# Kernel tuning notes

Measured on AMD Instinct MI355X. Metric: run time of the kernel, lower is better.

Reference implementation:

```python
import jax, jax.numpy as jnp
import numpy as np

DIM = 1024
NUM_HEADS = 16
HEAD_DIM = DIM // NUM_HEADS
SCALE = HEAD_DIM ** -0.5


def setup_inputs() -> dict:
    key = jax.random.key(0)
    ks = jax.random.split(key, 7)
    b, n = 2, 2048
    x = jax.random.normal(ks[0], (b, n, DIM), dtype=jnp.float32)
    s = DIM ** -0.5
    Wq = jax.random.normal(ks[1], (DIM, DIM), dtype=jnp.float32) * s
    bq = jax.random.normal(ks[2], (DIM,), dtype=jnp.float32) * 0.01
    Wk = jax.random.normal(ks[3], (DIM, DIM), dtype=jnp.float32) * s
    bk = jax.random.normal(ks[4], (DIM,), dtype=jnp.float32) * 0.01
    Wv = jax.random.normal(ks[5], (DIM, DIM), dtype=jnp.float32) * s
    bv = jax.random.normal(ks[6], (DIM,), dtype=jnp.float32) * 0.01
    return {"x": x, "Wq": Wq, "bq": bq, "Wk": Wk, "bk": bk, "Wv": Wv, "bv": bv}


def reference(x, Wq, bq, Wk, bk, Wv, bv):
    b, n, _ = x.shape
    # Linear projections (torch Linear: x @ W.T + b; here W stored as [in, out])
    q = x @ Wq + bq
    k = x @ Wk + bk
    v = x @ Wv + bv
    # split heads: [b, n, h*d] -> [b, h, n, d]
    split = lambda t: t.reshape(b, n, NUM_HEADS, HEAD_DIM).transpose(0, 2, 1, 3)
    q, k, v = split(q), split(k), split(v)
    sim = jnp.einsum('bhid,bhjd->bhij', q, k) * SCALE
    attn = jax.nn.softmax(sim, axis=-1)
    out = jnp.einsum('bhij,bhjd->bhid', attn, v)
    return out.transpose(0, 2, 1, 3).reshape(b, n, DIM)
```

## Files before the change

### kernel.cpp

```cpp
#include <hip/hip_runtime.h>
#include <cstdint>
#include <cstddef>

#define NB    2
#define SEQ   2048
#define DIMC  1024
#define NH    16
#define HDIM  64
#define MROWS (NB*SEQ)
#define NFEAT (3*DIMC)
#define KVBLK 64
#define NT    (SEQ/KVBLK)

typedef _Float16 half8 __attribute__((ext_vector_type(8)));
typedef _Float16 half4 __attribute__((ext_vector_type(4)));
typedef _Float16 half2v __attribute__((ext_vector_type(2)));
typedef __fp16   fp16x2 __attribute__((ext_vector_type(2)));
typedef float    f32x4 __attribute__((ext_vector_type(4)));

typedef const __attribute__((address_space(1))) void* gas_ptr;
typedef __attribute__((address_space(3))) void*       las_ptr;

__device__ __forceinline__ void gload_lds16(const void* g, void* l) {
    __builtin_amdgcn_global_load_lds((gas_ptr)g, (las_ptr)l, 16, 0, 0);
}

__device__ __forceinline__ int swz4(int r) { return (r ^ (r >> 2)) & 3; }

__device__ __forceinline__ float fast_exp2(float x) {
    float r;
    asm("v_exp_f32 %0, %1" : "=v"(r) : "v"(x));
    return r;
}

__device__ __forceinline__ half2v pk_f16(float a, float b) {
    fp16x2 r = __builtin_amdgcn_cvt_pkrtz(a, b);
    return __builtin_bit_cast(half2v, r);
}

__global__ __launch_bounds__(256) void k_convert_x(const float* __restrict__ x,
                                                   _Float16* __restrict__ x16) {
    int i = (blockIdx.x * 256 + threadIdx.x) * 4;
    float4 v = *reinterpret_cast<const float4*>(x + i);
    half4 h = { (_Float16)v.x, (_Float16)v.y, (_Float16)v.z, (_Float16)v.w };
    *reinterpret_cast<half4*>(x16 + i) = h;
}

__global__ __launch_bounds__(256) void k_transpose_w(const float* __restrict__ Wq,
                                                     const float* __restrict__ Wk,
                                                     const float* __restrict__ Wv,
                                                     _Float16* __restrict__ wt) {
    __shared__ float tile[64][65];
    const int bid  = blockIdx.x;
    const int midx = bid >> 8;
    const int t2   = bid & 255;
    const int i0   = (t2 >> 4) * 64;
    const int o0   = (t2 & 15) * 64;
    const float* W = (midx == 0) ? Wq : (midx == 1 ? Wk : Wv);
    const int tid  = threadIdx.x;
    #pragma unroll
    for (int p = 0; p < 4; ++p) {
        int id = p * 256 + tid;
        int r = id >> 4, c4 = (id & 15) * 4;
        float4 v = *reinterpret_cast<const float4*>(W + (size_t)(i0 + r) * DIMC + o0 + c4);
        tile[r][c4 + 0] = v.x; tile[r][c4 + 1] = v.y;
        tile[r][c4 + 2] = v.z; tile[r][c4 + 3] = v.w;
    }
    __syncthreads();
    #pragma unroll
    for (int p = 0; p < 4; ++p) {
        int id = p * 256 + tid;
        int oc = id >> 4, i4 = (id & 15) * 4;
        half4 h = { (_Float16)tile[i4 + 0][oc], (_Float16)tile[i4 + 1][oc],
                    (_Float16)tile[i4 + 2][oc], (_Float16)tile[i4 + 3][oc] };
        *reinterpret_cast<half4*>(wt + (size_t)(midx * DIMC + o0 + oc) * DIMC + i0 + i4) = h;
    }
}

__global__ __launch_bounds__(256) void k_qkv_gemm(
    const _Float16* __restrict__ x16, const _Float16* __restrict__ wt,
    const float* __restrict__ bq, const float* __restrict__ bk, const float* __restrict__ bv,
    _Float16* __restrict__ q16, _Float16* __restrict__ k16, _Float16* __restrict__ vt16)
{
    __shared__ __align__(16) char sraw[34816];
    const int tid = threadIdx.x;
    const int lane = tid & 63;
    const int w = tid >> 6, wm = w >> 1, wn = w & 1;
    const int lr = lane & 15, lg = lane >> 4;
    const int bn = blockIdx.x % (NFEAT / 128);
    const int bm = blockIdx.x / (NFEAT / 128);
    const int m0 = bm * 128, n0 = bn * 128;

    const f32x4 zero4 = {0.f, 0.f, 0.f, 0.f};
    f32x4 acc[4][4];
    #pragma unroll
    for (int i = 0; i < 4; ++i)
        #pragma unroll
        for (int j = 0; j < 4; ++j) acc[i][j] = zero4;

    auto stage = [&](int buf, int kt) {
        const int k0 = kt * 32;
        char* Adst = sraw + buf * 8192;
        char* Bdst = sraw + 16384 + buf * 8192;
        #pragma unroll
        for (int t = 0; t < 2; ++t) {
            int slot = t * 256 + tid;
            int row = slot >> 2, ch = slot & 3;
            int chg = ch ^ swz4(row);
            gload_lds16(x16 + (size_t)(m0 + row) * DIMC + k0 + chg * 8, Adst + slot * 16);
            gload_lds16(wt  + (size_t)(n0 + row) * DIMC + k0 + chg * 8, Bdst + slot * 16);
        }
    };

    stage(0, 0);
    for (int kt = 0; kt < DIMC / 32; ++kt) {
        __syncthreads();
        if (kt + 1 < DIMC / 32) stage((kt + 1) & 1, kt + 1);
        const char* Ab = sraw + (kt & 1) * 8192;
        const char* Bb = sraw + 16384 + (kt & 1) * 8192;
        half8 af[4], bf[4];
        #pragma unroll
        for (int mb = 0; mb < 4; ++mb) {
            int row = wm * 64 + mb * 16 + lr;
            af[mb] = *(const half8*)(Ab + row * 64 + ((lg ^ swz4(row)) << 4));
        }
        #pragma unroll
        for (int nb = 0; nb < 4; ++nb) {
            int col = wn * 64 + nb * 16 + lr;
            bf[nb] = *(const half8*)(Bb + col * 64 + ((lg ^ swz4(col)) << 4));
        }
        #pragma unroll
        for (int mb = 0; mb < 4; ++mb)
            #pragma unroll
            for (int nb = 0; nb < 4; ++nb)
                acc[mb][nb] = __builtin_amdgcn_mfma_f32_16x16x32_f16(af[mb], bf[nb], acc[mb][nb], 0, 0, 0);
    }

    const int sec = n0 >> 10;
    const float* bias = (sec == 0) ? bq : (sec == 1 ? bk : bv);
    const float scl = (sec == 0) ? 0.125f * 1.44269504088896f : 1.0f;
    float bfv[4];
    #pragma unroll
    for (int nb = 0; nb < 4; ++nb)
        bfv[nb] = bias[(n0 & 1023) + wn * 64 + nb * 16 + lr];

    if (sec < 2) {
        _Float16* dst = (sec == 0) ? q16 : k16;
        #pragma unroll
        for (int mb = 0; mb < 4; ++mb)
            #pragma unroll
            for (int i2 = 0; i2 < 4; ++i2) {
                int rg = m0 + wm * 64 + mb * 16 + lg * 4 + i2;
                int bb = rg >> 11, nn = rg & (SEQ - 1);
                #pragma unroll
                for (int nb = 0; nb < 4; ++nb) {
                    int f1 = (n0 & 1023) + wn * 64 + nb * 16 + lr;
                    int hh = f1 >> 6, dd = f1 & 63;
                    dst[((size_t)(bb * NH + hh) * SEQ + nn) * HDIM + dd] =
                        (_Float16)((acc[mb][nb][i2] + bfv[nb]) * scl);
                }
            }
    } else {
        __syncthreads();
        char* lt = sraw;
        #pragma unroll
        for (int mb = 0; mb < 4; ++mb)
            #pragma unroll
            for (int nb = 0; nb < 4; ++nb) {
                int c  = wn * 64 + nb * 16 + lr;
                int r0 = wm * 64 + mb * 16 + lg * 4;
                half4 hv = { (_Float16)(acc[mb][nb][0] + bfv[nb]),
                             (_Float16)(acc[mb][nb][1] + bfv[nb]),
                             (_Float16)(acc[mb][nb][2] + bfv[nb]),
                             (_Float16)(acc[mb][nb][3] + bfv[nb]) };
                *(half4*)(lt + c * 272 + r0 * 2) = hv;
            }
        __syncthreads();
        #pragma unroll
        for (int p = 0; p < 8; ++p) {
            int id = p * 256 + tid;
            int c = id >> 4, r8 = (id & 15) * 8;
            half8 hv = *(const half8*)(lt + c * 272 + r8 * 2);
            int f1 = (n0 & 1023) + c;
            int hh = f1 >> 6, dd = f1 & 63;
            int rg = m0 + r8;
            int bb = rg >> 11, nn = rg & (SEQ - 1);
            *(half8*)(vt16 + ((size_t)(bb * NH + hh) * HDIM + dd) * SEQ + nn) = hv;
        }
    }
}

__global__ __launch_bounds__(256) void k_attn(
    const _Float16* __restrict__ q16, const _Float16* __restrict__ k16,
    const _Float16* __restrict__ vt16, float* __restrict__ out)
{
    __shared__ __align__(16) char lds[49152];
    const int tid = threadIdx.x, lane = tid & 63, w = tid >> 6;
    const int lr = lane & 15, lg = lane >> 4;
    const int swz = (blockIdx.x & 7) * 64 + (blockIdx.x >> 3);
    const int bh = swz >> 4;
    const int qt = swz & 15;
    const int qrow0 = qt * 128 + w * 32;
    const _Float16* qh = q16 + (size_t)bh * SEQ * HDIM;
    const _Float16* kh = k16 + (size_t)bh * SEQ * HDIM;
    const _Float16* vh = vt16 + (size_t)bh * HDIM * SEQ;
    char* pl = lds + 32768 + w * 4096;
    const int rb = lr >> 3;

    auto stageKV = [&](int buf, int j0) {
        #pragma unroll
        for (int t = 0; t < 2; ++t) {
            int slot = t * 256 + tid;
            int row  = slot >> 3;
            int chg  = (slot & 7) ^ (row & 7);
            gload_lds16(kh + (size_t)(j0 + row) * HDIM + chg * 8,
                        lds + buf * 8192 + slot * 16);
            gload_lds16(vh + (size_t)row * SEQ + j0 + chg * 8,
                        lds + 16384 + buf * 8192 + slot * 16);
        }
    };

    half8 aq[2][2];
    #pragma unroll
    for (int g = 0; g < 2; ++g)
        #pragma unroll
        for (int kc = 0; kc < 2; ++kc)
            aq[g][kc] = *(const half8*)(qh + (size_t)(qrow0 + g * 16 + lr) * HDIM + kc * 32 + lg * 8);

    const f32x4 zero4 = {0.f, 0.f, 0.f, 0.f};
    f32x4 l4[2] = { zero4, zero4 };
    f32x4 oacc[2][4];
    #pragma unroll
    for (int g = 0; g < 2; ++g)
        #pragma unroll
        for (int i = 0; i < 4; ++i) oacc[g][i] = zero4;

    stageKV(0, 0);
    for (int t = 0; t < NT; ++t) {
        const int j0 = t * KVBLK;
        __syncthreads();
        if (t + 1 < NT) stageKV((t + 1) & 1, j0 + KVBLK);
        const char* Kb = lds + (t & 1) * 8192;
        const char* Vb = lds + 16384 + (t & 1) * 8192;

        f32x4 s[2][4];
        __builtin_amdgcn_s_setprio(1);
        #pragma unroll
        for (int jb = 0; jb < 4; ++jb) {
            int row = jb * 16 + lr;
            half8 k0 = *(const half8*)(Kb + row * 128 + (((0 + lg) ^ (row & 7)) << 4));
            half8 k1 = *(const half8*)(Kb + row * 128 + (((4 + lg) ^ (row & 7)) << 4));
            f32x4 sa0 = zero4, sa1 = zero4;
            sa0 = __builtin_amdgcn_mfma_f32_16x16x32_f16(k0, aq[0][0], sa0, 0, 0, 0);
            sa1 = __builtin_amdgcn_mfma_f32_16x16x32_f16(k0, aq[1][0], sa1, 0, 0, 0);
            sa0 = __builtin_amdgcn_mfma_f32_16x16x32_f16(k1, aq[0][1], sa0, 0, 0, 0);
            sa1 = __builtin_amdgcn_mfma_f32_16x16x32_f16(k1, aq[1][1], sa1, 0, 0, 0);
            s[0][jb] = sa0; s[1][jb] = sa1;
        }
        __builtin_amdgcn_s_setprio(0);

        half8 vf[4][2];
        #pragma unroll
        for (int db = 0; db < 4; ++db)
            #pragma unroll
            for (int kc = 0; kc < 2; ++kc) {
                int row = db * 16 + lr;
                vf[db][kc] = *(const half8*)(Vb + row * 128 + (((kc * 4 + lg) ^ (row & 7)) << 4));
            }

        #pragma unroll
        for (int g = 0; g < 2; ++g) {
            char* plg = pl + g * 2048;
            #pragma unroll
            for (int jb = 0; jb < 4; ++jb) {
                #pragma unroll
                for (int i = 0; i < 4; ++i)
                    s[g][jb][i] = fast_exp2(s[g][jb][i]);
                l4[g] += s[g][jb];
                half2v w0 = pk_f16(s[g][jb][0], s[g][jb][1]);
                half2v w1 = pk_f16(s[g][jb][2], s[g][jb][3]);
                half4 pk = { w0.x, w0.y, w1.x, w1.y };
                *(half4*)(plg + lr * 128 + (((jb * 2 + (lg >> 1)) ^ (lr & 7)) << 4)
                          + (((lg & 1) ^ rb) << 3)) = pk;
            }
        }
        asm volatile("s_waitcnt lgkmcnt(0)" ::: "memory");

        half8 ap[2][2];
        #pragma unroll
        for (int g = 0; g < 2; ++g) {
            const char* prow = pl + g * 2048 + lr * 128;
            half4 l0 = *(const half4*)(prow + (((0 + lg) ^ (lr & 7)) << 4) + (rb << 3));
            half4 h0 = *(const half4*)(prow + (((0 + lg) ^ (lr & 7)) << 4) + ((1 ^ rb) << 3));
            half4 l1 = *(const half4*)(prow + (((4 + lg) ^ (lr & 7)) << 4) + (rb << 3));
            half4 h1 = *(const half4*)(prow + (((4 + lg) ^ (lr & 7)) << 4) + ((1 ^ rb) << 3));
            ap[g][0] = half8{ l0.x, l0.y, l0.z, l0.w, h0.x, h0.y, h0.z, h0.w };
            ap[g][1] = half8{ l1.x, l1.y, l1.z, l1.w, h1.x, h1.y, h1.z, h1.w };
        }
        __builtin_amdgcn_s_setprio(1);
        #pragma unroll
        for (int db = 0; db < 4; ++db)
            #pragma unroll
            for (int g = 0; g < 2; ++g) {
                oacc[g][db] = __builtin_amdgcn_mfma_f32_16x16x32_f16(ap[g][0], vf[db][0], oacc[g][db], 0, 0, 0);
                oacc[g][db] = __builtin_amdgcn_mfma_f32_16x16x32_f16(ap[g][1], vf[db][1], oacc[g][db], 0, 0, 0);
            }
        __builtin_amdgcn_s_setprio(0);
    }

    const int bb = bh >> 4, hh = bh & 15;
    #pragma unroll
    for (int g = 0; g < 2; ++g) {
        float l_i = (l4[g][0] + l4[g][1]) + (l4[g][2] + l4[g][3]);
        l_i += __shfl_xor(l_i, 16);
        l_i += __shfl_xor(l_i, 32);
        float rlq[4];
        #pragma unroll
        for (int i = 0; i < 4; ++i)
            rlq[i] = 1.0f / __shfl(l_i, lg * 4 + i);
        #pragma unroll
        for (int db = 0; db < 4; ++db)
            #pragma unroll
            for (int i = 0; i < 4; ++i) {
                int nn = qrow0 + g * 16 + lg * 4 + i;
                out[((size_t)bb * SEQ + nn) * DIMC + hh * HDIM + db * 16 + lr] = oacc[g][db][i] * rlq[i];
            }
    }
}

extern "C" void kernel_launch(void* const* d_in, const int* in_sizes, int n_in,
                              void* d_out, int out_size, void* d_ws, size_t ws_size,
                              hipStream_t stream)
{
    const float* x  = (const float*)d_in[0];
    const float* Wq = (const float*)d_in[1];
    const float* bq = (const float*)d_in[2];
    const float* Wk = (const float*)d_in[3];
    const float* bk = (const float*)d_in[4];
    const float* Wv = (const float*)d_in[5];
    const float* bv = (const float*)d_in[6];
    float* out = (float*)d_out;

    char* ws = (char*)d_ws;
    _Float16* x16  = (_Float16*)ws;
    _Float16* wt   = (_Float16*)(ws + ((size_t)8  << 20));
    _Float16* q16  = (_Float16*)(ws + ((size_t)14 << 20));
    _Float16* k16  = (_Float16*)(ws + ((size_t)22 << 20));
    _Float16* vt16 = (_Float16*)(ws + ((size_t)30 << 20));

    k_convert_x<<<MROWS * DIMC / 1024, 256, 0, stream>>>(x, x16);
    k_transpose_w<<<3 * 256, 256, 0, stream>>>(Wq, Wk, Wv, wt);
    k_qkv_gemm<<<(MROWS / 128) * (NFEAT / 128), 256, 0, stream>>>(x16, wt, bq, bk, bv,
                                                                  q16, k16, vt16);
    k_attn<<<32 * (SEQ / 128), 256, 0, stream>>>(q16, k16, vt16, out);
}
```

Baseline: 99.42 us.

## Split attention KV range across two wave groups and triple-buffer QKV GEMM

The attention kernel now runs 512 threads per block: two groups of four waves each process half of the key/value sequence for the same query tile, then merge their partial outputs and row sums through LDS before normalizing. This doubles the parallelism per query tile, aiming to hide latency and use more waves. It costs more LDS, an extra reduction step and a serialized reuse of the P scratch buffer. The QKV GEMM moves from double to triple buffering, with explicit vmcnt waits and a raw barrier, so more global loads are in flight.

```diff
diff --git a/kernel.cpp b/kernel.cpp
--- a/kernel.cpp
+++ b/kernel.cpp
@@ -82,7 +82,7 @@
     const float* __restrict__ bq, const float* __restrict__ bk, const float* __restrict__ bv,
     _Float16* __restrict__ q16, _Float16* __restrict__ k16, _Float16* __restrict__ vt16)
 {
-    __shared__ __align__(16) char sraw[34816];
+    __shared__ __align__(16) char sraw[49152];
     const int tid = threadIdx.x;
     const int lane = tid & 63;
     const int w = tid >> 6, wm = w >> 1, wn = w & 1;
@@ -101,7 +101,7 @@
     auto stage = [&](int buf, int kt) {
         const int k0 = kt * 32;
         char* Adst = sraw + buf * 8192;
-        char* Bdst = sraw + 16384 + buf * 8192;
+        char* Bdst = sraw + 24576 + buf * 8192;
         #pragma unroll
         for (int t = 0; t < 2; ++t) {
             int slot = t * 256 + tid;
@@ -113,11 +113,14 @@
     };
 
     stage(0, 0);
+    stage(1, 1);
     for (int kt = 0; kt < DIMC / 32; ++kt) {
-        __syncthreads();
-        if (kt + 1 < DIMC / 32) stage((kt + 1) & 1, kt + 1);
-        const char* Ab = sraw + (kt & 1) * 8192;
-        const char* Bb = sraw + 16384 + (kt & 1) * 8192;
+        if (kt < DIMC / 32 - 1) asm volatile("s_waitcnt vmcnt(4)" ::: "memory");
+        else                    asm volatile("s_waitcnt vmcnt(0)" ::: "memory");
+        __builtin_amdgcn_s_barrier();
+        if (kt + 2 < DIMC / 32) stage((kt + 2) % 3, kt + 2);
+        const char* Ab = sraw + (kt % 3) * 8192;
+        const char* Bb = sraw + 24576 + (kt % 3) * 8192;
         half8 af[4], bf[4];
         #pragma unroll
         for (int mb = 0; mb < 4; ++mb) {
@@ -190,34 +193,38 @@
     }
 }
 
-__global__ __launch_bounds__(256) void k_attn(
+__global__ __launch_bounds__(512, 4) void k_attn(
     const _Float16* __restrict__ q16, const _Float16* __restrict__ k16,
     const _Float16* __restrict__ vt16, float* __restrict__ out)
 {
-    __shared__ __align__(16) char lds[49152];
+    __shared__ __align__(16) char lds[81920];
     const int tid = threadIdx.x, lane = tid & 63, w = tid >> 6;
     const int lr = lane & 15, lg = lane >> 4;
+    const int sub = w >> 2;
+    const int qg  = w & 3;
     const int swz = (blockIdx.x & 7) * 64 + (blockIdx.x >> 3);
     const int bh = swz >> 4;
     const int qt = swz & 15;
-    const int qrow0 = qt * 128 + w * 32;
+    const int qrow0 = qt * 128 + qg * 32;
     const _Float16* qh = q16 + (size_t)bh * SEQ * HDIM;
     const _Float16* kh = k16 + (size_t)bh * SEQ * HDIM;
     const _Float16* vh = vt16 + (size_t)bh * HDIM * SEQ;
-    char* pl = lds + 32768 + w * 4096;
+    char* pl = lds + 65536 + w * 2048;
     const int rb = lr >> 3;
 
-    auto stageKV = [&](int buf, int j0) {
-        #pragma unroll
-        for (int t = 0; t < 2; ++t) {
-            int slot = t * 256 + tid;
-            int row  = slot >> 3;
-            int chg  = (slot & 7) ^ (row & 7);
-            gload_lds16(kh + (size_t)(j0 + row) * HDIM + chg * 8,
-                        lds + buf * 8192 + slot * 16);
-            gload_lds16(vh + (size_t)row * SEQ + j0 + chg * 8,
-                        lds + 16384 + buf * 8192 + slot * 16);
-        }
+    const int srow = tid >> 3;
+    const int scg  = (tid & 7) ^ (srow & 7);
+
+    auto stageKV = [&](int buf, int t) {
+        const int jA = t * KVBLK, jB = (16 + t) * KVBLK;
+        gload_lds16(kh + (size_t)(jA + srow) * HDIM + scg * 8,
+                    lds + buf * 8192 + tid * 16);
+        gload_lds16(kh + (size_t)(jB + srow) * HDIM + scg * 8,
+                    lds + 16384 + buf * 8192 + tid * 16);
+        gload_lds16(vh + (size_t)srow * SEQ + jA + scg * 8,
+                    lds + 32768 + buf * 8192 + tid * 16);
+        gload_lds16(vh + (size_t)srow * SEQ + jB + scg * 8,
+                    lds + 49152 + buf * 8192 + tid * 16);
     };
 
     half8 aq[2][2];
@@ -236,95 +243,127 @@
         for (int i = 0; i < 4; ++i) oacc[g][i] = zero4;
 
     stageKV(0, 0);
-    for (int t = 0; t < NT; ++t) {
-        const int j0 = t * KVBLK;
+    for (int t = 0; t < 16; ++t) {
         __syncthreads();
-        if (t + 1 < NT) stageKV((t + 1) & 1, j0 + KVBLK);
-        const char* Kb = lds + (t & 1) * 8192;
-        const char* Vb = lds + 16384 + (t & 1) * 8192;
-
-        f32x4 s[2][4];
+        if (t + 1 < 16) stageKV((t + 1) & 1, t + 1);
+        const char* Kb = lds + sub * 16384 + (t & 1) * 8192;
+        const char* Vb = lds + 32768 + sub * 16384 + (t & 1) * 8192;
+
+        f32x4 s0[4], s1[4];
         __builtin_amdgcn_s_setprio(1);
         #pragma unroll
         for (int jb = 0; jb < 4; ++jb) {
             int row = jb * 16 + lr;
             half8 k0 = *(const half8*)(Kb + row * 128 + (((0 + lg) ^ (row & 7)) << 4));
             half8 k1 = *(const half8*)(Kb + row * 128 + (((4 + lg) ^ (row & 7)) << 4));
-            f32x4 sa0 = zero4, sa1 = zero4;
-            sa0 = __builtin_amdgcn_mfma_f32_16x16x32_f16(k0, aq[0][0], sa0, 0, 0, 0);
-            sa1 = __builtin_amdgcn_mfma_f32_16x16x32_f16(k0, aq[1][0], sa1, 0, 0, 0);
-            sa0 = __builtin_amdgcn_mfma_f32_16x16x32_f16(k1, aq[0][1], sa0, 0, 0, 0);
-            sa1 = __builtin_amdgcn_mfma_f32_16x16x32_f16(k1, aq[1][1], sa1, 0, 0, 0);
-            s[0][jb] = sa0; s[1][jb] = sa1;
+            f32x4 a0 = __builtin_amdgcn_mfma_f32_16x16x32_f16(k0, aq[0][0], zero4, 0, 0, 0);
+            f32x4 a1 = __builtin_amdgcn_mfma_f32_16x16x32_f16(k0, aq[1][0], zero4, 0, 0, 0);
+            a0 = __builtin_amdgcn_mfma_f32_16x16x32_f16(k1, aq[0][1], a0, 0, 0, 0);
+            a1 = __builtin_amdgcn_mfma_f32_16x16x32_f16(k1, aq[1][1], a1, 0, 0, 0);
+            s0[jb] = a0; s1[jb] = a1;
         }
         __builtin_amdgcn_s_setprio(0);
 
-        half8 vf[4][2];
-        #pragma unroll
-        for (int db = 0; db < 4; ++db)
-            #pragma unroll
-            for (int kc = 0; kc < 2; ++kc) {
-                int row = db * 16 + lr;
-                vf[db][kc] = *(const half8*)(Vb + row * 128 + (((kc * 4 + lg) ^ (row & 7)) << 4));
-            }
-
-        #pragma unroll
-        for (int g = 0; g < 2; ++g) {
-            char* plg = pl + g * 2048;
-            #pragma unroll
-            for (int jb = 0; jb < 4; ++jb) {
-                #pragma unroll
-                for (int i = 0; i < 4; ++i)
-                    s[g][jb][i] = fast_exp2(s[g][jb][i]);
-                l4[g] += s[g][jb];
-                half2v w0 = pk_f16(s[g][jb][0], s[g][jb][1]);
-                half2v w1 = pk_f16(s[g][jb][2], s[g][jb][3]);
-                half4 pk = { w0.x, w0.y, w1.x, w1.y };
-                *(half4*)(plg + lr * 128 + (((jb * 2 + (lg >> 1)) ^ (lr & 7)) << 4)
-                          + (((lg & 1) ^ rb) << 3)) = pk;
-            }
+        #pragma unroll
+        for (int jb = 0; jb < 4; ++jb) {
+            #pragma unroll
+            for (int i = 0; i < 4; ++i) s0[jb][i] = fast_exp2(s0[jb][i]);
+            l4[0] += s0[jb];
+            half2v w0 = pk_f16(s0[jb][0], s0[jb][1]);
+            half2v w1 = pk_f16(s0[jb][2], s0[jb][3]);
+            half4 pk = { w0.x, w0.y, w1.x, w1.y };
+            *(half4*)(pl + lr * 128 + (((jb * 2 + (lg >> 1)) ^ (lr & 7)) << 4)
+                      + (((lg & 1) ^ rb) << 3)) = pk;
+        }
+        half4 pk1[4];
+        #pragma unroll
+        for (int jb = 0; jb < 4; ++jb) {
+            #pragma unroll
+            for (int i = 0; i < 4; ++i) s1[jb][i] = fast_exp2(s1[jb][i]);
+            l4[1] += s1[jb];
+            half2v w0 = pk_f16(s1[jb][0], s1[jb][1]);
+            half2v w1 = pk_f16(s1[jb][2], s1[jb][3]);
+            pk1[jb] = half4{ w0.x, w0.y, w1.x, w1.y };
         }
         asm volatile("s_waitcnt lgkmcnt(0)" ::: "memory");
-
+        const char* prow = pl + lr * 128;
         half8 ap[2][2];
-        #pragma unroll
-        for (int g = 0; g < 2; ++g) {
-            const char* prow = pl + g * 2048 + lr * 128;
+        {
             half4 l0 = *(const half4*)(prow + (((0 + lg) ^ (lr & 7)) << 4) + (rb << 3));
             half4 h0 = *(const half4*)(prow + (((0 + lg) ^ (lr & 7)) << 4) + ((1 ^ rb) << 3));
             half4 l1 = *(const half4*)(prow + (((4 + lg) ^ (lr & 7)) << 4) + (rb << 3));
             half4 h1 = *(const half4*)(prow + (((4 + lg) ^ (lr & 7)) << 4) + ((1 ^ rb) << 3));
-            ap[g][0] = half8{ l0.x, l0.y, l0.z, l0.w, h0.x, h0.y, h0.z, h0.w };
-            ap[g][1] = half8{ l1.x, l1.y, l1.z, l1.w, h1.x, h1.y, h1.z, h1.w };
+            ap[0][0] = half8{ l0.x, l0.y, l0.z, l0.w, h0.x, h0.y, h0.z, h0.w };
+            ap[0][1] = half8{ l1.x, l1.y, l1.z, l1.w, h1.x, h1.y, h1.z, h1.w };
+        }
+        #pragma unroll
+        for (int jb = 0; jb < 4; ++jb)
+            *(half4*)(pl + lr * 128 + (((jb * 2 + (lg >> 1)) ^ (lr & 7)) << 4)
+                      + (((lg & 1) ^ rb) << 3)) = pk1[jb];
+        asm volatile("s_waitcnt lgkmcnt(0)" ::: "memory");
+        {
+            half4 l0 = *(const half4*)(prow + (((0 + lg) ^ (lr & 7)) << 4) + (rb << 3));
+            half4 h0 = *(const half4*)(prow + (((0 + lg) ^ (lr & 7)) << 4) + ((1 ^ rb) << 3));
+            half4 l1 = *(const half4*)(prow + (((4 + lg) ^ (lr & 7)) << 4) + (rb << 3));
+            half4 h1 = *(const half4*)(prow + (((4 + lg) ^ (lr & 7)) << 4) + ((1 ^ rb) << 3));
+            ap[1][0] = half8{ l0.x, l0.y, l0.z, l0.w, h0.x, h0.y, h0.z, h0.w };
+            ap[1][1] = half8{ l1.x, l1.y, l1.z, l1.w, h1.x, h1.y, h1.z, h1.w };
         }
         __builtin_amdgcn_s_setprio(1);
         #pragma unroll
-        for (int db = 0; db < 4; ++db)
-            #pragma unroll
-            for (int g = 0; g < 2; ++g) {
-                oacc[g][db] = __builtin_amdgcn_mfma_f32_16x16x32_f16(ap[g][0], vf[db][0], oacc[g][db], 0, 0, 0);
-                oacc[g][db] = __builtin_amdgcn_mfma_f32_16x16x32_f16(ap[g][1], vf[db][1], oacc[g][db], 0, 0, 0);
-            }
+        for (int db = 0; db < 4; ++db) {
+            int row = db * 16 + lr;
+            half8 vf0 = *(const half8*)(Vb + row * 128 + (((0 + lg) ^ (row & 7)) << 4));
+            half8 vf1 = *(const half8*)(Vb + row * 128 + (((4 + lg) ^ (row & 7)) << 4));
+            oacc[0][db] = __builtin_amdgcn_mfma_f32_16x16x32_f16(ap[0][0], vf0, oacc[0][db], 0, 0, 0);
+            oacc[1][db] = __builtin_amdgcn_mfma_f32_16x16x32_f16(ap[1][0], vf0, oacc[1][db], 0, 0, 0);
+            oacc[0][db] = __builtin_amdgcn_mfma_f32_16x16x32_f16(ap[0][1], vf1, oacc[0][db], 0, 0, 0);
+            oacc[1][db] = __builtin_amdgcn_mfma_f32_16x16x32_f16(ap[1][1], vf1, oacc[1][db], 0, 0, 0);
+        }
         __builtin_amdgcn_s_setprio(0);
     }
 
-    const int bb = bh >> 4, hh = bh & 15;
-    #pragma unroll
-    for (int g = 0; g < 2; ++g) {
-        float l_i = (l4[g][0] + l4[g][1]) + (l4[g][2] + l4[g][3]);
-        l_i += __shfl_xor(l_i, 16);
-        l_i += __shfl_xor(l_i, 32);
-        float rlq[4];
-        #pragma unroll
-        for (int i = 0; i < 4; ++i)
-            rlq[i] = 1.0f / __shfl(l_i, lg * 4 + i);
-        #pragma unroll
-        for (int db = 0; db < 4; ++db)
-            #pragma unroll
-            for (int i = 0; i < 4; ++i) {
-                int nn = qrow0 + g * 16 + lg * 4 + i;
-                out[((size_t)bb * SEQ + nn) * DIMC + hh * HDIM + db * 16 + lr] = oacc[g][db][i] * rlq[i];
-            }
+    __syncthreads();
+    char* xch = lds;
+    if (sub == 1) {
+        char* sl = xch + (qg * 2) * 5120;
+        #pragma unroll
+        for (int g = 0; g < 2; ++g) {
+            #pragma unroll
+            for (int db = 0; db < 4; ++db)
+                *(f32x4*)(sl + g * 5120 + db * 1024 + lane * 16) = oacc[g][db];
+            *(f32x4*)(sl + g * 5120 + 4096 + lane * 16) = l4[g];
+        }
+    }
+    __syncthreads();
+    if (sub == 0) {
+        char* sl = xch + (qg * 2) * 5120;
+        #pragma unroll
+        for (int g = 0; g < 2; ++g) {
+            #pragma unroll
+            for (int db = 0; db < 4; ++db)
+                oacc[g][db] += *(const f32x4*)(sl + g * 5120 + db * 1024 + lane * 16);
+            l4[g] += *(const f32x4*)(sl + g * 5120 + 4096 + lane * 16);
+        }
+        const int bb = bh >> 4, hh = bh & 15;
+        #pragma unroll
+        for (int g = 0; g < 2; ++g) {
+            float l_i = (l4[g][0] + l4[g][1]) + (l4[g][2] + l4[g][3]);
+            l_i += __shfl_xor(l_i, 16);
+            l_i += __shfl_xor(l_i, 32);
+            float rlq[4];
+            #pragma unroll
+            for (int i = 0; i < 4; ++i)
+                rlq[i] = 1.0f / __shfl(l_i, lg * 4 + i);
+            #pragma unroll
+            for (int db = 0; db < 4; ++db)
+                #pragma unroll
+                for (int i = 0; i < 4; ++i) {
+                    int nn = qrow0 + g * 16 + lg * 4 + i;
+                    out[((size_t)bb * SEQ + nn) * DIMC + hh * HDIM + db * 16 + lr] =
+                        oacc[g][db][i] * rlq[i];
+                }
+        }
     }
 }
 
@@ -352,5 +391,5 @@
     k_transpose_w<<<3 * 256, 256, 0, stream>>>(Wq, Wk, Wv, wt);
     k_qkv_gemm<<<(MROWS / 128) * (NFEAT / 128), 256, 0, stream>>>(x16, wt, bq, bk, bv,
                                                                   q16, k16, vt16);
-    k_attn<<<32 * (SEQ / 128), 256, 0, stream>>>(q16, k16, vt16, out);
-}
+    k_attn<<<32 * (SEQ / 128), 512, 0, stream>>>(q16, k16, vt16, out);
+}
```

After: 92.62 us. 1.07x faster.
